# Kernel tuning notes

Hardware: AMD Instinct MI355X
Metric: run time of the kernel (lower is better)

The kernel has to match this reference:

```python
import jax, jax.numpy as jnp
import numpy as np

B, N, D, S, ITERS = 32, 4096, 256, 7, 3
EPS_LN = 1e-5

def _ln(x, g, b):
    m = jnp.mean(x, axis=-1, keepdims=True)
    v = jnp.mean((x - m) ** 2, axis=-1, keepdims=True)
    return g * (x - m) * jax.lax.rsqrt(v + EPS_LN) + b

def setup_inputs() -> dict:
    key = jax.random.key(0)
    ks = jax.random.split(key, 16)
    w = lambda k, shape: (jax.random.normal(k, shape, jnp.float32) * 0.02)
    return {
        "inputs": jax.random.normal(ks[0], (B, N, D), jnp.float32),
        "noise": jax.random.normal(ks[1], (B, S, D), jnp.float32),
        "ln_in_g": jnp.ones((D,), jnp.float32), "ln_in_b": jnp.zeros((D,), jnp.float32),
        "ln_slots_g": jnp.ones((D,), jnp.float32), "ln_slots_b": jnp.zeros((D,), jnp.float32),
        "ln_mlp_g": jnp.ones((D,), jnp.float32), "ln_mlp_b": jnp.zeros((D,), jnp.float32),
        "slots_mu": w(ks[2], (1, 1, D)),
        "slots_sigma": jnp.ones((1, 1, D), jnp.float32),
        "wq": w(ks[3], (D, D)), "bq": jnp.zeros((D,), jnp.float32),
        "wk": w(ks[4], (D, D)), "bk": jnp.zeros((D,), jnp.float32),
        "wv": w(ks[5], (D, D)), "bv": jnp.zeros((D,), jnp.float32),
        "w_ih": w(ks[6], (3 * D, D)), "b_ih": jnp.zeros((3 * D,), jnp.float32),
        "w_hh": w(ks[7], (3 * D, D)), "b_hh": jnp.zeros((3 * D,), jnp.float32),
        "w1": w(ks[8], (2 * D, D)), "b1": jnp.zeros((2 * D,), jnp.float32),
        "w2": w(ks[9], (D, 2 * D)), "b2": jnp.zeros((D,), jnp.float32),
    }

def reference(inputs, noise, ln_in_g, ln_in_b, ln_slots_g, ln_slots_b, ln_mlp_g, ln_mlp_b,
              slots_mu, slots_sigma, wq, bq, wk, bk, wv, bv,
              w_ih, b_ih, w_hh, b_hh, w1, b1, w2, b2):
    x = _ln(inputs, ln_in_g, ln_in_b)                      # [B,N,D]
    sigma = jax.nn.softplus(slots_sigma)
    slots = slots_mu + sigma * noise                       # [B,S,D]
    k = x @ wk.T + bk                                      # [B,N,D]
    v = x @ wv.T + bv                                      # [B,N,D]
    scale = D ** -0.5
    attn = None
    for _ in range(ITERS):
        slots_prev = slots
        q = _ln(slots, ln_slots_g, ln_slots_b) @ wq.T + bq  # [B,S,D]
        logits = jnp.einsum('bsd,bnd->bsn', q, k) * scale   # [B,S,N]
        attn = jax.nn.softmax(logits, axis=1) + 1e-8        # softmax over slots
        attn = attn / jnp.sum(attn, axis=-1, keepdims=True)
        updates = jnp.einsum('bsn,bnd->bsd', attn, v)       # [B,S,D]
        # GRUCell(updates, slots_prev), torch gate order (r, z, n)
        gi = updates @ w_ih.T + b_ih                        # [B,S,3D]
        gh = slots_prev @ w_hh.T + b_hh
        i_r, i_z, i_n = jnp.split(gi, 3, axis=-1)
        h_r, h_z, h_n = jnp.split(gh, 3, axis=-1)
        r = jax.nn.sigmoid(i_r + h_r)
        z = jax.nn.sigmoid(i_z + h_z)
        n = jnp.tanh(i_n + r * h_n)
        slots = (1.0 - z) * n + z * slots_prev
        h = jax.nn.relu(_ln(slots, ln_mlp_g, ln_mlp_b) @ w1.T + b1)
        slots = slots + h @ w2.T + b2
    return slots, jnp.swapaxes(attn, 1, 2)                 # [B,S,D], [B,N,S]
```

## Files before the change

kernel.cpp:

```cpp
#include <hip/hip_runtime.h>
#include <stdint.h>

typedef unsigned short u16;
typedef unsigned int u32;
typedef float f32x4 __attribute__((ext_vector_type(4)));
typedef short short8 __attribute__((ext_vector_type(8)));

#define NBAT 32
#define NSEQ 4096
#define ND 256
#define NSLOT 7

__device__ __forceinline__ u32 bf16rne(float f){
  u32 u = __float_as_uint(f);
  u = u + 0x7FFFu + ((u >> 16) & 1u);
  return u >> 16;
}
__device__ __forceinline__ u32 packbf(float a, float b){
  return (bf16rne(a) & 0xFFFFu) | (bf16rne(b) << 16);
}
__device__ __forceinline__ float bflo(u32 u){ return __uint_as_float(u << 16); }
__device__ __forceinline__ float bfhi(u32 u){ return __uint_as_float(u & 0xFFFF0000u); }

__device__ __forceinline__ void gld16(void* lds, const void* g){
  __builtin_amdgcn_global_load_lds(
      (const __attribute__((address_space(1))) u32*)g,
      (__attribute__((address_space(3))) u32*)lds, 16, 0, 0);
}

__device__ __forceinline__ void softmax7(const float* z, float* p){
  float m = fmaxf(fmaxf(fmaxf(z[0], z[1]), fmaxf(z[2], z[3])),
                  fmaxf(fmaxf(z[4], z[5]), z[6]));
  float sum = 0.f;
#pragma unroll
  for (int s = 0; s < 7; ++s){ p[s] = exp2f(z[s] - m); sum += p[s]; }
  float r = 1.f / sum;
#pragma unroll
  for (int s = 0; s < 7; ++s) p[s] = fmaf(p[s], r, 1e-8f);
}

__global__ __launch_bounds__(256) void k_prep(
    const float* __restrict__ wk, const float* __restrict__ wv,
    const float* __restrict__ bk, const float* __restrict__ bv,
    const float* __restrict__ mu, const float* __restrict__ sig,
    const float* __restrict__ noise,
    const float* __restrict__ w_ih, const float* __restrict__ b_ih,
    const float* __restrict__ w_hh, const float* __restrict__ b_hh,
    const float* __restrict__ w1, const float* __restrict__ w2,
    const float* __restrict__ wq,
    u16* __restrict__ Wkv, float* __restrict__ biaskv, float* __restrict__ slots,
    u16* __restrict__ Wg, u16* __restrict__ w1b, u16* __restrict__ w2b,
    u16* __restrict__ wqb, float* __restrict__ bg){
  const int bid = blockIdx.x, t = threadIdx.x;
  if (bid < 512){
    const float* src = (bid < 256) ? (wk + (size_t)bid*256) : (wv + (size_t)(bid-256)*256);
    Wkv[(size_t)bid*256 + t] = (u16)bf16rne(src[t]);
  } else if (bid == 512){
    biaskv[t] = bk[t];
    biaskv[256 + t] = bv[t];
  } else if (bid < 737){
    int r = bid - 513;
    float sp = logf(1.f + expf(sig[t]));
    slots[(size_t)r*256 + t] = mu[t] + sp * noise[(size_t)r*256 + t];
  } else if (bid < 1761){
    int j = bid - 737;
    u16 a, b;
    if (j < 512){ a = (u16)bf16rne(w_ih[(size_t)j*256 + t]); b = (u16)bf16rne(w_hh[(size_t)j*256 + t]); }
    else if (j < 768){ a = (u16)bf16rne(w_ih[(size_t)j*256 + t]); b = 0; }
    else { a = 0; b = (u16)bf16rne(w_hh[(size_t)(j-256)*256 + t]); }
    Wg[(size_t)j*512 + t] = a;
    Wg[(size_t)j*512 + 256 + t] = b;
  } else if (bid < 2273){
    int j = bid - 1761;
    w1b[(size_t)j*256 + t] = (u16)bf16rne(w1[(size_t)j*256 + t]);
  } else if (bid < 2529){
    int j = bid - 2273;
    w2b[(size_t)j*512 + t]       = (u16)bf16rne(w2[(size_t)j*512 + t]);
    w2b[(size_t)j*512 + 256 + t] = (u16)bf16rne(w2[(size_t)j*512 + 256 + t]);
  } else if (bid < 2785){
    int j = bid - 2529;
    wqb[(size_t)j*256 + t] = (u16)bf16rne(wq[(size_t)j*256 + t]);
  } else {
#pragma unroll
    for (int ii = 0; ii < 4; ++ii){
      int j = ii*256 + t;
      float v;
      if (j < 512) v = b_ih[j] + b_hh[j];
      else if (j < 768) v = b_ih[j];
      else v = b_hh[j - 256];
      bg[j] = v;
    }
  }
}

__global__ __launch_bounds__(256) void k_ln_in(
    const float* __restrict__ x, const float* __restrict__ g, const float* __restrict__ b,
    u16* __restrict__ xo){
  const int row = blockIdx.x*4 + (threadIdx.x >> 6);
  const int lane = threadIdx.x & 63;
  const f32x4 v = *(const f32x4*)(x + (size_t)row*ND + lane*4);
  float s  = v[0]+v[1]+v[2]+v[3];
  float s2 = v[0]*v[0]+v[1]*v[1]+v[2]*v[2]+v[3]*v[3];
#pragma unroll
  for (int m = 1; m < 64; m <<= 1){ s += __shfl_xor(s, m); s2 += __shfl_xor(s2, m); }
  const float mean = s * (1.f/256.f);
  const float var  = s2 * (1.f/256.f) - mean*mean;
  const float rstd = rsqrtf(var + 1e-5f);
  const f32x4 gg = *(const f32x4*)(g + lane*4);
  const f32x4 bb = *(const f32x4*)(b + lane*4);
  float y0 = (v[0]-mean)*rstd*gg[0] + bb[0];
  float y1 = (v[1]-mean)*rstd*gg[1] + bb[1];
  float y2 = (v[2]-mean)*rstd*gg[2] + bb[2];
  float y3 = (v[3]-mean)*rstd*gg[3] + bb[3];
  uint2 o; o.x = packbf(y0, y1); o.y = packbf(y2, y3);
  *(uint2*)(xo + (size_t)row*ND + lane*4) = o;
}

__global__ __launch_bounds__(256) void k_gemm_kv(
    const u16* __restrict__ X, const u16* __restrict__ W,
    const float* __restrict__ biaskv, u16* __restrict__ kv){
  __shared__ __align__(16) u16 At[128*64];
  __shared__ __align__(16) u16 Bt[128*64];
  const int nb = blockIdx.x, mb = blockIdx.y;
  const int tid = threadIdx.x, w = tid >> 6, lane = tid & 63;
  const int wm = w >> 1, wn = w & 1;
  f32x4 acc[4][4];
#pragma unroll
  for (int a = 0; a < 4; ++a)
#pragma unroll
    for (int c = 0; c < 4; ++c) acc[a][c] = (f32x4){0.f,0.f,0.f,0.f};

  const int cl = lane & 7;
  for (int kt = 0; kt < 4; ++kt){
#pragma unroll
    for (int i = 0; i < 4; ++i){
      int R = w*32 + i*8 + (lane >> 3);
      int c = cl ^ (R & 7);
      gld16(&At[(w*32 + i*8)*64], X + ((size_t)(mb*128 + R))*256 + kt*64 + c*8);
      gld16(&Bt[(w*32 + i*8)*64], W + ((size_t)(nb*128 + R))*256 + kt*64 + c*8);
    }
    __syncthreads();
#pragma unroll
    for (int kk = 0; kk < 2; ++kk){
      short8 xf[4], wf[4];
#pragma unroll
      for (int xi = 0; xi < 4; ++xi){
        int r = wm*64 + xi*16 + (lane & 15);
        int ch = (kk*4 + (lane >> 4)) ^ (r & 7);
        xf[xi] = *(const short8*)&At[r*64 + ch*8];
      }
#pragma unroll
      for (int wi = 0; wi < 4; ++wi){
        int r = wn*64 + wi*16 + (lane & 15);
        int ch = (kk*4 + (lane >> 4)) ^ (r & 7);
        wf[wi] = *(const short8*)&Bt[r*64 + ch*8];
      }
#pragma unroll
      for (int xi = 0; xi < 4; ++xi)
#pragma unroll
        for (int wi = 0; wi < 4; ++wi)
          acc[xi][wi] = __builtin_amdgcn_mfma_f32_16x16x32_bf16(wf[wi], xf[xi], acc[xi][wi], 0, 0, 0);
    }
    __syncthreads();
  }
  f32x4 bias[4];
#pragma unroll
  for (int wi = 0; wi < 4; ++wi)
    bias[wi] = *(const f32x4*)(biaskv + nb*128 + wn*64 + wi*16 + (lane >> 4)*4);
#pragma unroll
  for (int xi = 0; xi < 4; ++xi){
    size_t m = (size_t)mb*128 + wm*64 + xi*16 + (lane & 15);
    u16* dst = kv + m*512 + nb*128 + wn*64 + (lane >> 4)*4;
#pragma unroll
    for (int wi = 0; wi < 4; ++wi){
      f32x4 c = acc[xi][wi];
      uint2 o;
      o.x = packbf(c[0] + bias[wi][0], c[1] + bias[wi][1]);
      o.y = packbf(c[2] + bias[wi][2], c[3] + bias[wi][3]);
      *(uint2*)(dst + wi*16) = o;
    }
  }
}

template<int MODE>
__global__ __launch_bounds__(256) void k_gemm_s(
    const u16* __restrict__ A, const u16* __restrict__ W,
    const float* __restrict__ bias, int nkt,
    float* __restrict__ outf, u16* __restrict__ outb,
    const float* __restrict__ snew, float* __restrict__ out2, int last){
  __shared__ __align__(16) u16 At[128*64];
  __shared__ __align__(16) u16 Bt[128*64];
  const int nb = blockIdx.x, mb = blockIdx.y;
  const int tid = threadIdx.x, w = tid >> 6, lane = tid & 63;
  const int wm = w >> 1, wn = w & 1;
  const size_t K = (size_t)nkt * 64;
  f32x4 acc[4][4];
#pragma unroll
  for (int a = 0; a < 4; ++a)
#pragma unroll
    for (int c = 0; c < 4; ++c) acc[a][c] = (f32x4){0.f,0.f,0.f,0.f};

  const int cl = lane & 7;
  for (int kt = 0; kt < nkt; ++kt){
#pragma unroll
    for (int i = 0; i < 4; ++i){
      int R = w*32 + i*8 + (lane >> 3);
      int c = cl ^ (R & 7);
      gld16(&At[(w*32 + i*8)*64], A + ((size_t)(mb*128 + R))*K + kt*64 + c*8);
      gld16(&Bt[(w*32 + i*8)*64], W + ((size_t)(nb*128 + R))*K + kt*64 + c*8);
    }
    __syncthreads();
#pragma unroll
    for (int kk = 0; kk < 2; ++kk){
      short8 xf[4], wf[4];
#pragma unroll
      for (int xi = 0; xi < 4; ++xi){
        int r = wm*64 + xi*16 + (lane & 15);
        int ch = (kk*4 + (lane >> 4)) ^ (r & 7);
        xf[xi] = *(const short8*)&At[r*64 + ch*8];
      }
#pragma unroll
      for (int wi = 0; wi < 4; ++wi){
        int r = wn*64 + wi*16 + (lane & 15);
        int ch = (kk*4 + (lane >> 4)) ^ (r & 7);
        wf[wi] = *(const short8*)&Bt[r*64 + ch*8];
      }
#pragma unroll
      for (int xi = 0; xi < 4; ++xi)
#pragma unroll
        for (int wi = 0; wi < 4; ++wi)
          acc[xi][wi] = __builtin_amdgcn_mfma_f32_16x16x32_bf16(wf[wi], xf[xi], acc[xi][wi], 0, 0, 0);
    }
    __syncthreads();
  }
  const int LDO = (MODE == 0) ? 1024 : ((MODE == 1) ? 512 : 256);
  f32x4 b4[4];
#pragma unroll
  for (int wi = 0; wi < 4; ++wi)
    b4[wi] = *(const f32x4*)(bias + nb*128 + wn*64 + wi*16 + (lane >> 4)*4);
#pragma unroll
  for (int xi = 0; xi < 4; ++xi){
    const int m = mb*128 + wm*64 + xi*16 + (lane & 15);
    const int colb = nb*128 + wn*64 + (lane >> 4)*4;
#pragma unroll
    for (int wi = 0; wi < 4; ++wi){
      const int col = colb + wi*16;
      f32x4 c = acc[xi][wi] + b4[wi];
      if (MODE == 0){
        *(f32x4*)(outf + (size_t)m*LDO + col) = c;
      } else if (MODE == 1){
        uint2 o;
        o.x = packbf(fmaxf(c[0],0.f), fmaxf(c[1],0.f));
        o.y = packbf(fmaxf(c[2],0.f), fmaxf(c[3],0.f));
        *(uint2*)(outb + (size_t)m*LDO + col) = o;
      } else if (MODE == 2){
        if (m < 224){
          const f32x4 s4 = *(const f32x4*)(snew + (size_t)m*256 + col);
          f32x4 o = c + s4;
          *(f32x4*)(outf + (size_t)m*LDO + col) = o;
          if (last) *(f32x4*)(out2 + (size_t)m*LDO + col) = o;
        }
      } else {
        f32x4 o = c * 0.09016844f;
        *(f32x4*)(outf + (size_t)m*LDO + col) = o;
      }
    }
  }
}

__global__ __launch_bounds__(256) void k_attn(
    const u16* __restrict__ kv, const float* __restrict__ qeff,
    float* __restrict__ attn_out, float* __restrict__ pacc, float* __restrict__ pw){
  __shared__ __align__(16) float accbuf[4][7][256];
  __shared__ float wsbuf[4][7];
  const int chunk = blockIdx.x, b = blockIdx.y;
  const int tid = threadIdx.x, w = tid >> 6, lane = tid & 63, hi = lane >> 5, lo = lane & 31;
  float qr[7][8];
  {
    const float* qb = qeff + (size_t)b*(NSLOT*256) + lo*8;
#pragma unroll
    for (int s = 0; s < 7; ++s){
      f32x4 q0 = *(const f32x4*)(qb + s*256);
      f32x4 q1 = *(const f32x4*)(qb + s*256 + 4);
      qr[s][0]=q0[0]; qr[s][1]=q0[1]; qr[s][2]=q0[2]; qr[s][3]=q0[3];
      qr[s][4]=q1[0]; qr[s][5]=q1[1]; qr[s][6]=q1[2]; qr[s][7]=q1[3];
    }
  }
  float acc[7][4]; float wsm[7];
#pragma unroll
  for (int s = 0; s < 7; ++s){ acc[s][0]=acc[s][1]=acc[s][2]=acc[s][3]=0.f; wsm[s]=0.f; }

  const size_t bbase = (size_t)b*NSEQ;
  for (int it = 0; it < 16; ++it){
    const int nr = chunk*128 + it*8 + w*2;
    const size_t rowm = (bbase + nr + hi)*512;
    const size_t rowo = (bbase + nr + (1 - hi))*512;
    uint4 k4 = *(const uint4*)(kv + rowm + lo*8);
    float kf[8];
    kf[0]=bflo(k4.x); kf[1]=bfhi(k4.x); kf[2]=bflo(k4.y); kf[3]=bfhi(k4.y);
    kf[4]=bflo(k4.z); kf[5]=bfhi(k4.z); kf[6]=bflo(k4.w); kf[7]=bfhi(k4.w);
    float z[7];
#pragma unroll
    for (int s = 0; s < 7; ++s){
      float d0 = fmaf(qr[s][0],kf[0], fmaf(qr[s][1],kf[1], fmaf(qr[s][2],kf[2], qr[s][3]*kf[3])));
      float d1 = fmaf(qr[s][4],kf[4], fmaf(qr[s][5],kf[5], fmaf(qr[s][6],kf[6], qr[s][7]*kf[7])));
      z[s] = d0 + d1;
    }
#pragma unroll
    for (int m = 1; m < 32; m <<= 1){
#pragma unroll
      for (int s = 0; s < 7; ++s) z[s] += __shfl_xor(z[s], m);
    }
    float zo[7];
#pragma unroll
    for (int s = 0; s < 7; ++s) zo[s] = __shfl_xor(z[s], 32);
    float pm[7], po[7];
    softmax7(z, pm);
    softmax7(zo, po);
    float sel = pm[0];
    sel = (lo==1)?pm[1]:sel; sel = (lo==2)?pm[2]:sel; sel = (lo==3)?pm[3]:sel;
    sel = (lo==4)?pm[4]:sel; sel = (lo==5)?pm[5]:sel; sel = (lo==6)?pm[6]:sel;
    if (lo < 7) attn_out[(bbase + nr + hi)*7 + lo] = sel;
    uint2 va = *(const uint2*)(kv + rowm + 256 + (size_t)lane*4);
    uint2 vb = *(const uint2*)(kv + rowo + 256 + (size_t)lane*4);
    float vm0=bflo(va.x), vm1=bfhi(va.x), vm2=bflo(va.y), vm3=bfhi(va.y);
    float vo0=bflo(vb.x), vo1=bfhi(vb.x), vo2=bflo(vb.y), vo3=bfhi(vb.y);
#pragma unroll
    for (int s = 0; s < 7; ++s){
      acc[s][0] = fmaf(pm[s], vm0, fmaf(po[s], vo0, acc[s][0]));
      acc[s][1] = fmaf(pm[s], vm1, fmaf(po[s], vo1, acc[s][1]));
      acc[s][2] = fmaf(pm[s], vm2, fmaf(po[s], vo2, acc[s][2]));
      acc[s][3] = fmaf(pm[s], vm3, fmaf(po[s], vo3, acc[s][3]));
      wsm[s] += pm[s] + po[s];
    }
  }
#pragma unroll
  for (int s = 0; s < 7; ++s)
    *(f32x4*)&accbuf[w][s][lane*4] = (f32x4){acc[s][0], acc[s][1], acc[s][2], acc[s][3]};
  if (lane == 0){
#pragma unroll
    for (int s = 0; s < 7; ++s) wsbuf[w][s] = wsm[s];
  }
  __syncthreads();
#pragma unroll
  for (int s = 0; s < 7; ++s){
    float sum = accbuf[0][s][tid] + accbuf[1][s][tid] + accbuf[2][s][tid] + accbuf[3][s][tid];
    pacc[((size_t)chunk*NBAT + b)*(NSLOT*256) + s*256 + tid] = sum;
  }
  if (tid < 7)
    pw[((size_t)chunk*NBAT + b)*NSLOT + tid] =
        wsbuf[0][tid] + wsbuf[1][tid] + wsbuf[2][tid] + wsbuf[3][tid];
}

__global__ __launch_bounds__(256) void k_slotA(
    const float* __restrict__ pacc, const float* __restrict__ pw,
    const float* __restrict__ slots, u16* __restrict__ A2, float* __restrict__ wsum){
  __shared__ float pwb[32];
  const int r = blockIdx.x, t = threadIdx.x;
  if (r >= 224){
    A2[(size_t)r*512 + t] = 0;
    A2[(size_t)r*512 + 256 + t] = 0;
    return;
  }
  if (t < 32) pwb[t] = pw[(size_t)t*224 + r];
  float u = 0.f;
#pragma unroll 8
  for (int c = 0; c < 32; ++c) u += pacc[(size_t)c*57344 + (size_t)r*256 + t];
  __syncthreads();
  float wst = 0.f;
#pragma unroll
  for (int c = 0; c < 32; ++c) wst += pwb[c];
  if (t == 0) wsum[r] = wst;
  A2[(size_t)r*512 + t] = (u16)bf16rne(u / wst);
  A2[(size_t)r*512 + 256 + t] = (u16)bf16rne(slots[(size_t)r*256 + t]);
}

__global__ __launch_bounds__(256) void k_slotB(
    const float* __restrict__ gates, const float* __restrict__ slots,
    const float* __restrict__ gm, const float* __restrict__ bm,
    float* __restrict__ snew, u16* __restrict__ lnm){
  __shared__ float red[8];
  const int r = blockIdx.x, t = threadIdx.x;
  if (r >= 224){ lnm[(size_t)r*256 + t] = 0; return; }
  const float g0  = gates[(size_t)r*1024 + t];
  const float g1  = gates[(size_t)r*1024 + 256 + t];
  const float gin = gates[(size_t)r*1024 + 512 + t];
  const float ghn = gates[(size_t)r*1024 + 768 + t];
  const float spv = slots[(size_t)r*256 + t];
  const float rr = 1.f/(1.f + __expf(-g0));
  const float zz = 1.f/(1.f + __expf(-g1));
  float xx = gin + rr*ghn;
  xx = fminf(fmaxf(xx, -15.f), 15.f);
  const float e2 = __expf(2.f*xx);
  const float nn = (e2 - 1.f)/(e2 + 1.f);
  const float sp = (1.f - zz)*nn + zz*spv;
  snew[(size_t)r*256 + t] = sp;
  float s = sp, s2 = sp*sp;
#pragma unroll
  for (int m = 1; m < 64; m <<= 1){ s += __shfl_xor(s, m); s2 += __shfl_xor(s2, m); }
  if ((t & 63) == 0){ red[t >> 6] = s; red[4 + (t >> 6)] = s2; }
  __syncthreads();
  const float ssum = red[0]+red[1]+red[2]+red[3];
  const float qsum = red[4]+red[5]+red[6]+red[7];
  const float mean = ssum*(1.f/256.f);
  const float var  = qsum*(1.f/256.f) - mean*mean;
  const float rstd = rsqrtf(var + 1e-5f);
  lnm[(size_t)r*256 + t] = (u16)bf16rne((sp - mean)*rstd*gm[t] + bm[t]);
}

__global__ __launch_bounds__(256) void k_lnq(
    const float* __restrict__ slots, const float* __restrict__ g, const float* __restrict__ b,
    u16* __restrict__ lnq){
  __shared__ float red[8];
  const int r = blockIdx.x, t = threadIdx.x;
  if (r >= 224){ lnq[(size_t)r*256 + t] = 0; return; }
  const float x = slots[(size_t)r*256 + t];
  float s = x, s2 = x*x;
#pragma unroll
  for (int m = 1; m < 64; m <<= 1){ s += __shfl_xor(s, m); s2 += __shfl_xor(s2, m); }
  if ((t & 63) == 0){ red[t >> 6] = s; red[4 + (t >> 6)] = s2; }
  __syncthreads();
  const float ssum = red[0]+red[1]+red[2]+red[3];
  const float qsum = red[4]+red[5]+red[6]+red[7];
  const float mean = ssum*(1.f/256.f);
  const float var  = qsum*(1.f/256.f) - mean*mean;
  const float rstd = rsqrtf(var + 1e-5f);
  lnq[(size_t)r*256 + t] = (u16)bf16rne((x - mean)*rstd*g[t] + b[t]);
}

__global__ __launch_bounds__(256) void k_norm(
    float* __restrict__ attn, const float* __restrict__ wsum_tot){
  size_t i = (size_t)blockIdx.x*256 + threadIdx.x;
  int s = (int)(i % 7);
  int b = (int)(i / (NSEQ*7));
  attn[i] = attn[i] / wsum_tot[b*7 + s];
}

extern "C" void kernel_launch(void* const* d_in, const int* in_sizes, int n_in,
                              void* d_out, int out_size, void* d_ws, size_t ws_size,
                              hipStream_t stream){
  (void)in_sizes; (void)n_in; (void)out_size; (void)ws_size;
  const float* inputs  = (const float*)d_in[0];
  const float* noise   = (const float*)d_in[1];
  const float* ln_in_g = (const float*)d_in[2];
  const float* ln_in_b = (const float*)d_in[3];
  const float* ln_sl_g = (const float*)d_in[4];
  const float* ln_sl_b = (const float*)d_in[5];
  const float* ln_ml_g = (const float*)d_in[6];
  const float* ln_ml_b = (const float*)d_in[7];
  const float* mu      = (const float*)d_in[8];
  const float* sig     = (const float*)d_in[9];
  const float* wq      = (const float*)d_in[10];
  const float* bq      = (const float*)d_in[11];
  const float* wk      = (const float*)d_in[12];
  const float* bk      = (const float*)d_in[13];
  const float* wv      = (const float*)d_in[14];
  const float* bv      = (const float*)d_in[15];
  const float* w_ih    = (const float*)d_in[16];
  const float* b_ih    = (const float*)d_in[17];
  const float* w_hh    = (const float*)d_in[18];
  const float* b_hh    = (const float*)d_in[19];
  const float* w1      = (const float*)d_in[20];
  const float* b1      = (const float*)d_in[21];
  const float* w2      = (const float*)d_in[22];
  const float* b2      = (const float*)d_in[23];

  char* ws = (char*)d_ws;
  u16*   x_bf   = (u16*)(ws);
  u16*   kv     = (u16*)(ws + 67108864);
  char*  paccch = ws + 201326592;
  float* pacc   = (float*)paccch;
  u16*   Wkv    = (u16*)(ws + 208666624);
  float* qeff   = (float*)(ws + 208928768);
  float* slots  = (float*)(ws + 209190912);
  float* pw     = (float*)(ws + 209420288);
  float* biaskv = (float*)(ws + 209448960);
  float* wsum   = (float*)(ws + 209451008);
  u16*   A2     = (u16*)(ws + 209452032);
  u16*   Wg     = (u16*)(ws + 209714176);
  u16*   w1b    = (u16*)(ws + 210762752);
  u16*   w2b    = (u16*)(ws + 211024896);
  u16*   wqb    = (u16*)(ws + 211287040);
  float* bg     = (float*)(ws + 211418112);

  float* gates  = (float*)(paccch);
  u16*   hb     = (u16*)(paccch + 1048576);
  u16*   lnm    = (u16*)(paccch + 1310720);
  u16*   lnq    = (u16*)(paccch + 1441792);
  float* snew   = (float*)(paccch + 1572864);

  float* out_slots = (float*)d_out;
  float* attn = (float*)d_out + 57344;

  k_prep<<<2786, 256, 0, stream>>>(wk, wv, bk, bv, mu, sig, noise,
                                   w_ih, b_ih, w_hh, b_hh, w1, w2, wq,
                                   Wkv, biaskv, slots, Wg, w1b, w2b, wqb, bg);
  k_ln_in<<<32768, 256, 0, stream>>>(inputs, ln_in_g, ln_in_b, x_bf);
  k_gemm_kv<<<dim3(4, 1024), 256, 0, stream>>>(x_bf, Wkv, biaskv, kv);
  for (int i = 0; i < 3; ++i){
    const int last = (i == 2) ? 1 : 0;
    k_lnq<<<256, 256, 0, stream>>>(slots, ln_sl_g, ln_sl_b, lnq);
    k_gemm_s<3><<<dim3(2, 2), 256, 0, stream>>>(lnq, wqb, bq, 4, qeff, nullptr, nullptr, nullptr, 0);
    k_attn<<<dim3(32, 32), 256, 0, stream>>>(kv, qeff, attn, pacc, pw);
    k_slotA<<<256, 256, 0, stream>>>(pacc, pw, slots, A2, wsum);
    k_gemm_s<0><<<dim3(8, 2), 256, 0, stream>>>(A2, Wg, bg, 8, gates, nullptr, nullptr, nullptr, 0);
    k_slotB<<<256, 256, 0, stream>>>(gates, slots, ln_ml_g, ln_ml_b, snew, lnm);
    k_gemm_s<1><<<dim3(4, 2), 256, 0, stream>>>(lnm, w1b, b1, 4, nullptr, hb, nullptr, nullptr, 0);
    k_gemm_s<2><<<dim3(2, 2), 256, 0, stream>>>(hb, w2b, b2, 8, slots, nullptr, snew, out_slots, last);
  }
  k_norm<<<3584, 256, 0, stream>>>(attn, wsum);
}
```

Measured before the change: 431.6 us.

## Double the attention chunk grid, prefetch K/V rows, and swizzle KV GEMM blocks

The attention kernel now splits each batch into 64 chunks of 64 rows instead of 32 chunks of 128. This doubles the grid to 2048 blocks, which should fill the GPU better. Inside each block, the K and V loads for the next row pair are issued one iteration ahead to hide global memory latency. The KV projection GEMM switches to a 1D grid with an XCD-style block swizzle so neighbouring blocks share data in L2. In exchange, the partial-sum buffer and the slotA reduction double in size, and the use of extra registers for prefetch may lower occupancy.

```diff
diff --git a/kernel.cpp b/kernel.cpp
--- a/kernel.cpp
+++ b/kernel.cpp
@@ -10,6 +10,7 @@
 #define NSEQ 4096
 #define ND 256
 #define NSLOT 7
+#define NCHUNK 64
 
 __device__ __forceinline__ u32 bf16rne(float f){
   u32 u = __float_as_uint(f);
@@ -121,7 +122,9 @@
     const float* __restrict__ biaskv, u16* __restrict__ kv){
   __shared__ __align__(16) u16 At[128*64];
   __shared__ __align__(16) u16 Bt[128*64];
-  const int nb = blockIdx.x, mb = blockIdx.y;
+  const int bid = blockIdx.x;
+  const int swz = ((bid & 7) << 9) + (bid >> 3);
+  const int mb = swz >> 2, nb = swz & 3;
   const int tid = threadIdx.x, w = tid >> 6, lane = tid & 63;
   const int wm = w >> 1, wn = w & 1;
   f32x4 acc[4][4];
@@ -291,11 +294,25 @@
   for (int s = 0; s < 7; ++s){ acc[s][0]=acc[s][1]=acc[s][2]=acc[s][3]=0.f; wsm[s]=0.f; }
 
   const size_t bbase = (size_t)b*NSEQ;
-  for (int it = 0; it < 16; ++it){
-    const int nr = chunk*128 + it*8 + w*2;
-    const size_t rowm = (bbase + nr + hi)*512;
-    const size_t rowo = (bbase + nr + (1 - hi))*512;
-    uint4 k4 = *(const uint4*)(kv + rowm + lo*8);
+  const int nr0 = chunk*64 + w*2;
+  uint4 k4; uint2 va, vb;
+  {
+    const size_t rowm = (bbase + nr0 + hi)*512;
+    const size_t rowo = (bbase + nr0 + (1 - hi))*512;
+    k4 = *(const uint4*)(kv + rowm + lo*8);
+    va = *(const uint2*)(kv + rowm + 256 + (size_t)lane*4);
+    vb = *(const uint2*)(kv + rowo + 256 + (size_t)lane*4);
+  }
+  for (int it = 0; it < 8; ++it){
+    const int nr = nr0 + it*8;
+    uint4 k4n; uint2 van, vbn;
+    if (it < 7){
+      const size_t rowmn = (bbase + nr + 8 + hi)*512;
+      const size_t rowon = (bbase + nr + 8 + (1 - hi))*512;
+      k4n = *(const uint4*)(kv + rowmn + lo*8);
+      van = *(const uint2*)(kv + rowmn + 256 + (size_t)lane*4);
+      vbn = *(const uint2*)(kv + rowon + 256 + (size_t)lane*4);
+    }
     float kf[8];
     kf[0]=bflo(k4.x); kf[1]=bfhi(k4.x); kf[2]=bflo(k4.y); kf[3]=bfhi(k4.y);
     kf[4]=bflo(k4.z); kf[5]=bfhi(k4.z); kf[6]=bflo(k4.w); kf[7]=bfhi(k4.w);
@@ -320,9 +337,7 @@
     float sel = pm[0];
     sel = (lo==1)?pm[1]:sel; sel = (lo==2)?pm[2]:sel; sel = (lo==3)?pm[3]:sel;
     sel = (lo==4)?pm[4]:sel; sel = (lo==5)?pm[5]:sel; sel = (lo==6)?pm[6]:sel;
-    if (lo < 7) attn_out[(bbase + nr + hi)*7 + lo] = sel;
-    uint2 va = *(const uint2*)(kv + rowm + 256 + (size_t)lane*4);
-    uint2 vb = *(const uint2*)(kv + rowo + 256 + (size_t)lane*4);
+    if (lo < 7) attn_out[((size_t)bbase + nr + hi)*7 + lo] = sel;
     float vm0=bflo(va.x), vm1=bfhi(va.x), vm2=bflo(va.y), vm3=bfhi(va.y);
     float vo0=bflo(vb.x), vo1=bfhi(vb.x), vo2=bflo(vb.y), vo3=bfhi(vb.y);
 #pragma unroll
@@ -333,6 +348,7 @@
       acc[s][3] = fmaf(pm[s], vm3, fmaf(po[s], vo3, acc[s][3]));
       wsm[s] += pm[s] + po[s];
     }
+    if (it < 7){ k4 = k4n; va = van; vb = vbn; }
   }
 #pragma unroll
   for (int s = 0; s < 7; ++s)
@@ -355,21 +371,21 @@
 __global__ __launch_bounds__(256) void k_slotA(
     const float* __restrict__ pacc, const float* __restrict__ pw,
     const float* __restrict__ slots, u16* __restrict__ A2, float* __restrict__ wsum){
-  __shared__ float pwb[32];
+  __shared__ float pwb[NCHUNK];
   const int r = blockIdx.x, t = threadIdx.x;
   if (r >= 224){
     A2[(size_t)r*512 + t] = 0;
     A2[(size_t)r*512 + 256 + t] = 0;
     return;
   }
-  if (t < 32) pwb[t] = pw[(size_t)t*224 + r];
+  if (t < NCHUNK) pwb[t] = pw[(size_t)t*224 + r];
   float u = 0.f;
 #pragma unroll 8
-  for (int c = 0; c < 32; ++c) u += pacc[(size_t)c*57344 + (size_t)r*256 + t];
+  for (int c = 0; c < NCHUNK; ++c) u += pacc[(size_t)c*57344 + (size_t)r*256 + t];
   __syncthreads();
   float wst = 0.f;
 #pragma unroll
-  for (int c = 0; c < 32; ++c) wst += pwb[c];
+  for (int c = 0; c < NCHUNK; ++c) wst += pwb[c];
   if (t == 0) wsum[r] = wst;
   A2[(size_t)r*512 + t] = (u16)bf16rne(u / wst);
   A2[(size_t)r*512 + 256 + t] = (u16)bf16rne(slots[(size_t)r*256 + t]);
@@ -470,18 +486,18 @@
   u16*   kv     = (u16*)(ws + 67108864);
   char*  paccch = ws + 201326592;
   float* pacc   = (float*)paccch;
-  u16*   Wkv    = (u16*)(ws + 208666624);
-  float* qeff   = (float*)(ws + 208928768);
-  float* slots  = (float*)(ws + 209190912);
-  float* pw     = (float*)(ws + 209420288);
-  float* biaskv = (float*)(ws + 209448960);
-  float* wsum   = (float*)(ws + 209451008);
-  u16*   A2     = (u16*)(ws + 209452032);
-  u16*   Wg     = (u16*)(ws + 209714176);
-  u16*   w1b    = (u16*)(ws + 210762752);
-  u16*   w2b    = (u16*)(ws + 211024896);
-  u16*   wqb    = (u16*)(ws + 211287040);
-  float* bg     = (float*)(ws + 211418112);
+  u16*   Wkv    = (u16*)(ws + 216006656);
+  float* qeff   = (float*)(ws + 216268800);
+  float* slots  = (float*)(ws + 216530944);
+  float* pw     = (float*)(ws + 216760320);
+  float* biaskv = (float*)(ws + 216817664);
+  float* wsum   = (float*)(ws + 216819712);
+  u16*   A2     = (u16*)(ws + 216820736);
+  u16*   Wg     = (u16*)(ws + 217082880);
+  u16*   w1b    = (u16*)(ws + 218131456);
+  u16*   w2b    = (u16*)(ws + 218393600);
+  u16*   wqb    = (u16*)(ws + 218655744);
+  float* bg     = (float*)(ws + 218786816);
 
   float* gates  = (float*)(paccch);
   u16*   hb     = (u16*)(paccch + 1048576);
@@ -496,12 +512,12 @@
                                    w_ih, b_ih, w_hh, b_hh, w1, w2, wq,
                                    Wkv, biaskv, slots, Wg, w1b, w2b, wqb, bg);
   k_ln_in<<<32768, 256, 0, stream>>>(inputs, ln_in_g, ln_in_b, x_bf);
-  k_gemm_kv<<<dim3(4, 1024), 256, 0, stream>>>(x_bf, Wkv, biaskv, kv);
+  k_gemm_kv<<<4096, 256, 0, stream>>>(x_bf, Wkv, biaskv, kv);
   for (int i = 0; i < 3; ++i){
     const int last = (i == 2) ? 1 : 0;
     k_lnq<<<256, 256, 0, stream>>>(slots, ln_sl_g, ln_sl_b, lnq);
     k_gemm_s<3><<<dim3(2, 2), 256, 0, stream>>>(lnq, wqb, bq, 4, qeff, nullptr, nullptr, nullptr, 0);
-    k_attn<<<dim3(32, 32), 256, 0, stream>>>(kv, qeff, attn, pacc, pw);
+    k_attn<<<dim3(NCHUNK, 32), 256, 0, stream>>>(kv, qeff, attn, pacc, pw);
     k_slotA<<<256, 256, 0, stream>>>(pacc, pw, slots, A2, wsum);
     k_gemm_s<0><<<dim3(8, 2), 256, 0, stream>>>(A2, Wg, bg, 8, gates, nullptr, nullptr, nullptr, 0);
     k_slotB<<<256, 256, 0, stream>>>(gates, slots, ln_ml_g, ln_ml_b, snew, lnm);
```

New measurement: 417.2 us. 1.03x faster.
